# Performance work log

Measured on AMD Instinct MI355X. Metric: run time of the kernel, lower is better.

The kernel has to match this reference:

```python
import jax, jax.numpy as jnp
import numpy as np
import math

D_EMB = 1024
N_HEADS = 16
SCALE = 0.02
B, T = 4, 2048


def _norm(x):
    # torch.std_mean default: unbiased std (ddof=1) over last dim
    m = jnp.mean(x, axis=-1, keepdims=True)
    s = jnp.std(x, axis=-1, keepdims=True, ddof=1)
    return (x - m) / (s + 1e-05)


def setup_inputs() -> dict:
    key = jax.random.key(0)
    kx, kw = jax.random.split(key)
    x = jax.random.normal(kx, (B, D_EMB, T), dtype=jnp.float32)
    qkv = jax.random.normal(kw, (3, N_HEADS, D_EMB, D_EMB // N_HEADS), dtype=jnp.float32) * SCALE
    return {"x": x, "qkv": qkv}


def reference(x, qkv):
    Bsz, D, Tlen = x.shape
    H = qkv.shape[1]
    # (3, B, H, T, d_head)
    h = jnp.einsum('bdt,nhde->nbhte', x, qkv)
    q, k, v = h[0], h[1], h[2]
    q = _norm(q)
    k = _norm(k)
    scale = math.sqrt(D // H)  # torch: sqrt(d_emb // H)
    attn = jnp.einsum('bhte,bhse->bhts', q, k) / scale  # [B,H,T,T]
    attn = jax.nn.softmax(attn, axis=-1)
    out = jnp.einsum('bhts,bhse->bhet', attn, v)  # [B,H,d_head,T]
    return out.reshape(Bsz, D, Tlen)
```

## Files before the change

kernel.cpp:

```cpp
#include <hip/hip_runtime.h>
#include <hip/hip_bf16.h>

#define B_SZ 4
#define NHEADS 16
#define T_SZ 2048
#define DE 1024
#define DH 64
#define BH (B_SZ*NHEADS)
#define SCL 0.18033688011112042f

typedef __attribute__((ext_vector_type(8))) short short8;
typedef __attribute__((ext_vector_type(4))) float float4v;
typedef __attribute__((ext_vector_type(16))) float f32x16;
typedef __attribute__((ext_vector_type(2))) unsigned int uint2v;
typedef __attribute__((ext_vector_type(4))) unsigned int uint4v;

__device__ __forceinline__ short f2bf(float f) {
    __hip_bfloat16 h = __float2bfloat16(f);
    return *reinterpret_cast<short*>(&h);
}
__device__ __forceinline__ unsigned int pack_bf2(float a, float b) {
    float2 f; f.x = a; f.y = b;
    __hip_bfloat162 h = __float22bfloat162_rn(f);
    return *reinterpret_cast<unsigned int*>(&h);
}
__device__ __forceinline__ float4v zero4() {
    float4v z = {0.f, 0.f, 0.f, 0.f};
    return z;
}
__device__ __forceinline__ int swz(int row, int g) {
    return row * 64 + (((g) ^ (row & 7)) << 3);
}
__device__ __forceinline__ void gl_lds16(const short* g, short* l) {
    __builtin_amdgcn_global_load_lds(
        (const __attribute__((address_space(1))) void*)g,
        (__attribute__((address_space(3))) void*)l, 16, 0, 0);
}

__global__ __launch_bounds__(256) void transpose_k(const float* __restrict__ src,
                                                   short* __restrict__ dst,
                                                   int R, int C) {
    __shared__ __align__(16) short tile[64 * 65];
    int c0 = blockIdx.x * 64, r0 = blockIdx.y * 64;
    src += (size_t)blockIdx.z * R * C;
    dst += (size_t)blockIdx.z * R * C;
    int tid = threadIdx.x;
#pragma unroll
    for (int it = 0; it < 16; ++it) {
        int idx = it * 256 + tid;
        int rr = idx >> 6, cc = idx & 63;
        tile[cc * 65 + rr] = f2bf(src[(size_t)(r0 + rr) * C + c0 + cc]);
    }
    __syncthreads();
#pragma unroll
    for (int it = 0; it < 16; ++it) {
        int idx = it * 256 + tid;
        int cc = idx >> 6, rr = idx & 63;
        dst[(size_t)(c0 + cc) * R + r0 + rr] = tile[cc * 65 + rr];
    }
}

__global__ __launch_bounds__(256, 2) void qkv_k(const short* __restrict__ XT,
                                                const short* __restrict__ WT,
                                                short* __restrict__ Qw,
                                                short* __restrict__ Kw,
                                                short* __restrict__ Vt) {
    __shared__ __align__(16) short ldsA[2][128 * 64];
    __shared__ __align__(16) short ldsB[2][128 * 64];
    int b  = blockIdx.x >> 4;
    int t0 = (blockIdx.x & 15) * 128;
    int n  = blockIdx.y >> 3;
    int h0 = (blockIdx.y & 7) * 2;
    int tid = threadIdx.x, wave = tid >> 6, lane = tid & 63;
    int l15 = lane & 15, quad = lane >> 4;
    int wr = wave >> 1, wc = wave & 1;

    const short* Arow = XT + ((size_t)b * T_SZ + t0) * DE;
    const short* Brow = WT + ((size_t)n * 1024 + h0 * 64) * DE;

    int rA = lane >> 3;
    int gl = (lane & 7) ^ rA;

    float4v acc[4][4];
#pragma unroll
    for (int mm = 0; mm < 4; ++mm)
#pragma unroll
        for (int j = 0; j < 4; ++j) acc[mm][j] = zero4();

    auto STAGE = [&](short* La, short* Lb, int k0) {
#pragma unroll
        for (int it = 0; it < 4; ++it) {
            int rowbase = it * 32 + wave * 8;
            gl_lds16(&Arow[(size_t)(rowbase + rA) * DE + k0 + gl * 8],
                     &La[(it * 256 + wave * 64) * 8]);
            gl_lds16(&Brow[(size_t)(rowbase + rA) * DE + k0 + gl * 8],
                     &Lb[(it * 256 + wave * 64) * 8]);
        }
    };
    auto COMPUTE = [&](const short* La, const short* Lb) {
#pragma unroll
        for (int ks = 0; ks < 2; ++ks) {
            short8 af[4], bf[4];
#pragma unroll
            for (int mm = 0; mm < 4; ++mm)
                af[mm] = *(const short8*)&La[swz(64 * wr + 16 * mm + l15, 4 * ks + quad)];
#pragma unroll
            for (int j = 0; j < 4; ++j)
                bf[j] = *(const short8*)&Lb[swz(64 * wc + 16 * j + l15, 4 * ks + quad)];
#pragma unroll
            for (int mm = 0; mm < 4; ++mm)
#pragma unroll
                for (int j = 0; j < 4; ++j)
                    acc[mm][j] = __builtin_amdgcn_mfma_f32_16x16x32_bf16(af[mm], bf[j], acc[mm][j], 0, 0, 0);
        }
    };

    STAGE(ldsA[0], ldsB[0], 0);
    __syncthreads();
    for (int k0 = 0; k0 < DE; k0 += 128) {
        STAGE(ldsA[1], ldsB[1], k0 + 64);
        COMPUTE(ldsA[0], ldsB[0]);
        __syncthreads();
        if (k0 + 128 < DE)
            STAGE(ldsA[0], ldsB[0], k0 + 128);
        COMPUTE(ldsA[1], ldsB[1]);
        __syncthreads();
    }

    int h = h0 + wc;
    int bh = b * NHEADS + h;
#pragma unroll
    for (int mm = 0; mm < 4; ++mm) {
        int tbase = t0 + 64 * wr + 16 * mm;
        if (n < 2) {
            float oscale = (n == 0) ? SCL : 1.0f;
            float mu[4], inv[4];
#pragma unroll
            for (int r = 0; r < 4; ++r) {
                float s1 = 0.f, s2 = 0.f;
#pragma unroll
                for (int jj = 0; jj < 4; ++jj) {
                    float v = acc[mm][jj][r];
                    s1 += v; s2 += v * v;
                }
                for (int sh = 1; sh < 16; sh <<= 1) {
                    s1 += __shfl_xor(s1, sh, 64);
                    s2 += __shfl_xor(s2, sh, 64);
                }
                mu[r] = s1 * (1.0f / 64.0f);
                float var = (s2 - 64.0f * mu[r] * mu[r]) * (1.0f / 63.0f);
                var = fmaxf(var, 0.0f);
                inv[r] = oscale / (sqrtf(var) + 1e-5f);
            }
            short* dst = (n == 0 ? Qw : Kw) + (size_t)bh * T_SZ * DH;
#pragma unroll
            for (int r = 0; r < 4; ++r) {
                int t = tbase + quad * 4 + r;
#pragma unroll
                for (int jj = 0; jj < 4; ++jj) {
                    float v = (acc[mm][jj][r] - mu[r]) * inv[r];
                    dst[(size_t)t * DH + 16 * jj + l15] = f2bf(v);
                }
            }
        } else {
#pragma unroll
            for (int r = 0; r < 4; ++r) {
                int t = tbase + quad * 4 + r;
#pragma unroll
                for (int jj = 0; jj < 4; ++jj) {
                    Vt[((size_t)bh * DH + 16 * jj + l15) * T_SZ + t] =
                        f2bf(acc[mm][jj][r]);
                }
            }
        }
    }
}

__global__ __launch_bounds__(256, 4) void attn_k(const short* __restrict__ Qw,
                                                 const short* __restrict__ Kw,
                                                 const short* __restrict__ Vt,
                                                 float* __restrict__ out) {
    __shared__ __align__(16) char smem[32768];
    short* ldsK = (short*)smem;
    short* ldsV = (short*)(smem + 16384);
    float* ldsL = (float*)smem;

    int bh = blockIdx.x;
    int t0 = blockIdx.y * 128;
    int b = bh >> 4, h = bh & 15;
    int tid = threadIdx.x, wave = tid >> 6, lane = tid & 63;
    int l31 = lane & 31, b5 = lane >> 5;
    int tw = t0 + 32 * wave;

    const short* Qp = Qw + (size_t)bh * T_SZ * DH;
    const short* Kp = Kw + (size_t)bh * T_SZ * DH;
    const short* Vp = Vt + (size_t)bh * DH * T_SZ;

    int rA = lane >> 3;
    int g8 = lane & 7;

    short8 qf[4];
#pragma unroll
    for (int kk = 0; kk < 4; ++kk)
        qf[kk] = *(const short8*)&Qp[(size_t)(tw + l31) * DH + 16 * kk + 8 * b5];

    f32x16 o0 = (f32x16)0.0f, o1 = (f32x16)0.0f;
    float ol = 0.f;

    short8 rk[2], rv[2];
    auto LOADNEXT = [&](int s) {
#pragma unroll
        for (int it = 0; it < 2; ++it) {
            int row = 16 * wave + 8 * it + rA;
            rk[it] = *(const short8*)&Kp[(size_t)(s + row) * DH + g8 * 8];
            rv[it] = *(const short8*)&Vp[(size_t)row * T_SZ + s + g8 * 8];
        }
    };
    auto WRITESTAGE = [&](int buf) {
        short* Kb = ldsK + buf * 4096;
        short* Vb = ldsV + buf * 4096;
#pragma unroll
        for (int it = 0; it < 2; ++it) {
            int row = 16 * wave + 8 * it + rA;
            *(short8*)&Kb[swz(row, g8)] = rk[it];
            *(short8*)&Vb[swz(row, g8)] = rv[it];
        }
    };

    LOADNEXT(0);
    WRITESTAGE(0);
    __syncthreads();

    for (int s0 = 0; s0 < T_SZ; s0 += 64) {
        int cur = (s0 >> 6) & 1;
        LOADNEXT((s0 + 64) & (T_SZ - 1));
        const short* Kc = ldsK + cur * 4096;
        const short* Vc = ldsV + cur * 4096;

        __builtin_amdgcn_s_setprio(1);

        uint2v u[2][4];
#pragma unroll
        for (int ss = 0; ss < 2; ++ss) {
            f32x16 z = (f32x16)0.0f;
#pragma unroll
            for (int kk = 0; kk < 4; ++kk) {
                short8 ak = *(const short8*)&Kc[swz(32 * ss + l31, 2 * kk + b5)];
                z = __builtin_amdgcn_mfma_f32_32x32x16_bf16(ak, qf[kk], z, 0, 0, 0);
            }
#pragma unroll
            for (int g = 0; g < 4; ++g) {
                float p0 = __builtin_amdgcn_exp2f(z[4 * g + 0]);
                float p1 = __builtin_amdgcn_exp2f(z[4 * g + 1]);
                float p2 = __builtin_amdgcn_exp2f(z[4 * g + 2]);
                float p3 = __builtin_amdgcn_exp2f(z[4 * g + 3]);
                ol += (p0 + p1) + (p2 + p3);
                u[ss][g].x = pack_bf2(p0, p1);
                u[ss][g].y = pack_bf2(p2, p3);
            }
        }

#pragma unroll
        for (int kks = 0; kks < 4; ++kks) {
            const int ssb = kks >> 1, ga = 2 * (kks & 1);
            unsigned a0 = u[ssb][ga].x,     a1 = u[ssb][ga].y;
            unsigned b0 = u[ssb][ga + 1].x, b1 = u[ssb][ga + 1].y;
            asm("v_permlane32_swap_b32 %0, %1" : "+v"(a0), "+v"(b0));
            asm("v_permlane32_swap_b32 %0, %1" : "+v"(a1), "+v"(b1));
            uint4v up; up.x = a0; up.y = a1; up.z = b0; up.w = b1;
            short8 pf = *(short8*)&up;
            short8 v0 = *(const short8*)&Vc[swz(l31, 2 * kks + b5)];
            short8 v1 = *(const short8*)&Vc[swz(32 + l31, 2 * kks + b5)];
            o0 = __builtin_amdgcn_mfma_f32_32x32x16_bf16(pf, v0, o0, 0, 0, 0);
            o1 = __builtin_amdgcn_mfma_f32_32x32x16_bf16(pf, v1, o1, 0, 0, 0);
        }

        __builtin_amdgcn_s_setprio(0);

        WRITESTAGE(cur ^ 1);
        __syncthreads();
    }

    {
        float l = ol + __shfl_xor(ol, 32, 64);
        if (lane < 32) ldsL[wave * 32 + lane] = 1.0f / l;
    }

#pragma unroll
    for (int g = 0; g < 4; ++g) {
        float4v ri = *(const float4v*)&ldsL[wave * 32 + 8 * g + 4 * b5];
        float4v ov;
#pragma unroll
        for (int i = 0; i < 4; ++i) ov[i] = o0[4 * g + i] * ri[i];
        *(float4v*)&out[(size_t)(b * DE + h * DH + l31) * T_SZ
                        + tw + 8 * g + 4 * b5] = ov;
#pragma unroll
        for (int i = 0; i < 4; ++i) ov[i] = o1[4 * g + i] * ri[i];
        *(float4v*)&out[(size_t)(b * DE + h * DH + 32 + l31) * T_SZ
                        + tw + 8 * g + 4 * b5] = ov;
    }
}

extern "C" void kernel_launch(void* const* d_in, const int* in_sizes, int n_in,
                              void* d_out, int out_size, void* d_ws, size_t ws_size,
                              hipStream_t stream) {
    const float* x = (const float*)d_in[0];
    const float* w = (const float*)d_in[1];
    float* out = (float*)d_out;
    char* ws = (char*)d_ws;

    const size_t XT_BYTES = (size_t)B_SZ * T_SZ * DE * 2;
    const size_t WT_BYTES = (size_t)3 * NHEADS * DH * DE * 2;
    const size_t QKV_BYTES = (size_t)BH * T_SZ * DH * 2;

    short* XT = (short*)(ws);
    short* WT = (short*)(ws + XT_BYTES);
    short* Qw = (short*)(ws + XT_BYTES + WT_BYTES);
    short* Kw = (short*)(ws + XT_BYTES + WT_BYTES + QKV_BYTES);
    short* Vt = (short*)(ws + XT_BYTES + WT_BYTES + 2 * QKV_BYTES);

    transpose_k<<<dim3(T_SZ / 64, DE / 64, B_SZ), 256, 0, stream>>>(x, XT, DE, T_SZ);
    transpose_k<<<dim3(1, DE / 64, 3 * NHEADS), 256, 0, stream>>>(w, WT, DE, DH);
    qkv_k<<<dim3(64, 24), 256, 0, stream>>>(XT, WT, Qw, Kw, Vt);
    attn_k<<<dim3(BH, T_SZ / 128), 256, 0, stream>>>(Qw, Kw, Vt, out);
}
```

Measured before the change: 246.7 us.

## Read K and V fragments directly from global memory instead of staging through LDS

Drops the double-buffered LDS staging of K and V tiles, the block-wide barriers and the priority hints. Each wave now loads its MFMA operand fragments for K and transposed V straight from global memory and relies on L1/L2 caching, since all four waves read the same tiles. This removes the LDS writes, reads and syncs, at the cost of repeated global loads with higher latency, no explicit prefetch, and less coalesced 16-byte accesses.

```diff
diff --git a/kernel.cpp b/kernel.cpp
--- a/kernel.cpp
+++ b/kernel.cpp
@@ -180,10 +180,7 @@
                                                  const short* __restrict__ Kw,
                                                  const short* __restrict__ Vt,
                                                  float* __restrict__ out) {
-    __shared__ __align__(16) char smem[32768];
-    short* ldsK = (short*)smem;
-    short* ldsV = (short*)(smem + 16384);
-    float* ldsL = (float*)smem;
+    __shared__ float ldsL[4][32];
 
     int bh = blockIdx.x;
     int t0 = blockIdx.y * 128;
@@ -196,9 +193,6 @@
     const short* Kp = Kw + (size_t)bh * T_SZ * DH;
     const short* Vp = Vt + (size_t)bh * DH * T_SZ;
 
-    int rA = lane >> 3;
-    int g8 = lane & 7;
-
     short8 qf[4];
 #pragma unroll
     for (int kk = 0; kk < 4; ++kk)
@@ -207,47 +201,16 @@
     f32x16 o0 = (f32x16)0.0f, o1 = (f32x16)0.0f;
     float ol = 0.f;
 
-    short8 rk[2], rv[2];
-    auto LOADNEXT = [&](int s) {
-#pragma unroll
-        for (int it = 0; it < 2; ++it) {
-            int row = 16 * wave + 8 * it + rA;
-            rk[it] = *(const short8*)&Kp[(size_t)(s + row) * DH + g8 * 8];
-            rv[it] = *(const short8*)&Vp[(size_t)row * T_SZ + s + g8 * 8];
-        }
-    };
-    auto WRITESTAGE = [&](int buf) {
-        short* Kb = ldsK + buf * 4096;
-        short* Vb = ldsV + buf * 4096;
-#pragma unroll
-        for (int it = 0; it < 2; ++it) {
-            int row = 16 * wave + 8 * it + rA;
-            *(short8*)&Kb[swz(row, g8)] = rk[it];
-            *(short8*)&Vb[swz(row, g8)] = rv[it];
-        }
-    };
-
-    LOADNEXT(0);
-    WRITESTAGE(0);
-    __syncthreads();
-
     for (int s0 = 0; s0 < T_SZ; s0 += 64) {
-        int cur = (s0 >> 6) & 1;
-        LOADNEXT((s0 + 64) & (T_SZ - 1));
-        const short* Kc = ldsK + cur * 4096;
-        const short* Vc = ldsV + cur * 4096;
-
-        __builtin_amdgcn_s_setprio(1);
-
-        uint2v u[2][4];
 #pragma unroll
         for (int ss = 0; ss < 2; ++ss) {
             f32x16 z = (f32x16)0.0f;
 #pragma unroll
             for (int kk = 0; kk < 4; ++kk) {
-                short8 ak = *(const short8*)&Kc[swz(32 * ss + l31, 2 * kk + b5)];
+                short8 ak = *(const short8*)&Kp[(size_t)(s0 + 32 * ss + l31) * DH + 16 * kk + 8 * b5];
                 z = __builtin_amdgcn_mfma_f32_32x32x16_bf16(ak, qf[kk], z, 0, 0, 0);
             }
+            uint2v u[4];
 #pragma unroll
             for (int g = 0; g < 4; ++g) {
                 float p0 = __builtin_amdgcn_exp2f(z[4 * g + 0]);
@@ -255,40 +218,35 @@
                 float p2 = __builtin_amdgcn_exp2f(z[4 * g + 2]);
                 float p3 = __builtin_amdgcn_exp2f(z[4 * g + 3]);
                 ol += (p0 + p1) + (p2 + p3);
-                u[ss][g].x = pack_bf2(p0, p1);
-                u[ss][g].y = pack_bf2(p2, p3);
-            }
-        }
-
-#pragma unroll
-        for (int kks = 0; kks < 4; ++kks) {
-            const int ssb = kks >> 1, ga = 2 * (kks & 1);
-            unsigned a0 = u[ssb][ga].x,     a1 = u[ssb][ga].y;
-            unsigned b0 = u[ssb][ga + 1].x, b1 = u[ssb][ga + 1].y;
-            asm("v_permlane32_swap_b32 %0, %1" : "+v"(a0), "+v"(b0));
-            asm("v_permlane32_swap_b32 %0, %1" : "+v"(a1), "+v"(b1));
-            uint4v up; up.x = a0; up.y = a1; up.z = b0; up.w = b1;
-            short8 pf = *(short8*)&up;
-            short8 v0 = *(const short8*)&Vc[swz(l31, 2 * kks + b5)];
-            short8 v1 = *(const short8*)&Vc[swz(32 + l31, 2 * kks + b5)];
-            o0 = __builtin_amdgcn_mfma_f32_32x32x16_bf16(pf, v0, o0, 0, 0, 0);
-            o1 = __builtin_amdgcn_mfma_f32_32x32x16_bf16(pf, v1, o1, 0, 0, 0);
-        }
-
-        __builtin_amdgcn_s_setprio(0);
-
-        WRITESTAGE(cur ^ 1);
-        __syncthreads();
+                u[g].x = pack_bf2(p0, p1);
+                u[g].y = pack_bf2(p2, p3);
+            }
+#pragma unroll
+            for (int kkh = 0; kkh < 2; ++kkh) {
+                const int ga = 2 * kkh;
+                unsigned a0 = u[ga].x,     a1 = u[ga].y;
+                unsigned b0 = u[ga + 1].x, b1 = u[ga + 1].y;
+                asm("v_permlane32_swap_b32 %0, %1" : "+v"(a0), "+v"(b0));
+                asm("v_permlane32_swap_b32 %0, %1" : "+v"(a1), "+v"(b1));
+                uint4v up; up.x = a0; up.y = a1; up.z = b0; up.w = b1;
+                short8 pf = *(short8*)&up;
+                const int sc = s0 + 16 * (2 * ss + kkh) + 8 * b5;
+                short8 v0 = *(const short8*)&Vp[(size_t)l31 * T_SZ + sc];
+                short8 v1 = *(const short8*)&Vp[(size_t)(32 + l31) * T_SZ + sc];
+                o0 = __builtin_amdgcn_mfma_f32_32x32x16_bf16(pf, v0, o0, 0, 0, 0);
+                o1 = __builtin_amdgcn_mfma_f32_32x32x16_bf16(pf, v1, o1, 0, 0, 0);
+            }
+        }
     }
 
     {
         float l = ol + __shfl_xor(ol, 32, 64);
-        if (lane < 32) ldsL[wave * 32 + lane] = 1.0f / l;
+        if (lane < 32) ldsL[wave][lane] = 1.0f / l;
     }
 
 #pragma unroll
     for (int g = 0; g < 4; ++g) {
-        float4v ri = *(const float4v*)&ldsL[wave * 32 + 8 * g + 4 * b5];
+        float4v ri = *(const float4v*)&ldsL[wave][8 * g + 4 * b5];
         float4v ov;
 #pragma unroll
         for (int i = 0; i < 4; ++i) ov[i] = o0[4 * g + i] * ri[i];
```

Result: slower. 404.6 us (+64.0%).
